# Performance work log

Hardware: AMD Instinct MI355X
Metric: run time of the kernel (lower is better)

The kernel has to match this reference:

```python
import jax, jax.numpy as jnp
import numpy as np

B, T, K = 64, 1024, 128
START, STOP = K - 2, K - 1  # tag_dictionary['<START>'], tag_dictionary['<STOP>']
NEG = -10000.0


def setup_inputs() -> dict:
    key = jax.random.key(0)
    k1, k2, k3, k4 = jax.random.split(key, 4)
    feats = jax.random.normal(k1, (B, T, K), jnp.float32)
    tags = jax.random.randint(k2, (B, T), 0, K - 2)          # real labels only
    lens = jax.random.randint(k3, (B,), 1, T + 1)            # 1 <= len <= T
    transitions = jax.random.normal(k4, (K, K), jnp.float32)
    transitions = transitions.at[START, :].set(NEG).at[:, STOP].set(NEG)
    return {"feats": feats, "tags": tags, "lens": lens, "transitions": transitions}


def _forward_alg(feats, transitions, lens):
    # feats: [B, T, K]; CRF forward (log-partition) via scan over time.
    B_, T_, K_ = feats.shape
    # init: only START position kept from feats[:, 0, :], rest -10000
    alpha0 = jnp.full((B_, K_), NEG, feats.dtype).at[:, START].set(feats[:, 0, START])

    def step(alpha, feat_i):
        # tag_var[b, s, p] = feat_i[b, s] + transitions[s, p] + alpha[b, p]
        new = feat_i + jax.scipy.special.logsumexp(alpha[:, None, :] + transitions[None, :, :], axis=2)
        return new, new

    _, alphas = jax.lax.scan(step, alpha0, jnp.swapaxes(feats[:, 1:, :], 0, 1))  # [T-1, B, K]
    all_alphas = jnp.concatenate([alpha0[None], alphas], axis=0)  # [T, B, K]; idx t-1 == forward_var[:, t]
    terminal = all_alphas[lens - 1, jnp.arange(B_)]               # [B, K]
    return jax.scipy.special.logsumexp(terminal, axis=1)          # [B]


def _score_sentence(feats, transitions, tags, lens):
    B_, T_, K_ = feats.shape
    pos = jnp.arange(T_ - 1)
    # pad_stop_tags = tags[:, 1:] with positions >= len-1 replaced by STOP
    stop_tags = jnp.where(pos[None, :] >= (lens - 1)[:, None], STOP, tags[:, 1:])
    trans_sc = transitions[stop_tags, tags[:, :-1]]               # [B, T-1]
    tmask = (pos[None, :] < (lens - 1)[:, None]).astype(feats.dtype)
    emit = jnp.take_along_axis(feats, tags[:, :, None], axis=2)[:, :, 0]  # [B, T]
    emask = (jnp.arange(T_)[None, :] < lens[:, None]).astype(feats.dtype)
    return jnp.sum(trans_sc * tmask, axis=1) + jnp.sum(emit * emask, axis=1)


def reference(feats, tags, lens, transitions):
    forward_score = _forward_alg(feats, transitions, lens)
    gold_score = _score_sentence(feats, transitions, tags, lens)
    return jnp.mean(forward_score - gold_score)
```

## Files before the change

kernel.cpp:

```cpp
#include <hip/hip_runtime.h>
#include <math.h>

#define BB 64
#define TT 1024
#define KK 128
#define START_TAG 126
#define STOP_TAG 127
#define NTHREADS 512
#define CS 64

typedef float v2f __attribute__((ext_vector_type(2)));

__global__ __launch_bounds__(NTHREADS) void crf_forward(
    const float* __restrict__ feats,
    const int*   __restrict__ tags,
    const int*   __restrict__ lens,
    const float* __restrict__ trans,
    float*       __restrict__ out_pb)
{
  __shared__ float Tld[KK][KK + 1];
  __shared__ __align__(16) float e_lds[KK];
  __shared__ float partial[NTHREADS];
  __shared__ float maxT_lds[KK];
  __shared__ __align__(16) float Fbuf[CS * KK];
  __shared__ float wsum[NTHREADS / 64];

  const int tid = threadIdx.x;
  const int b   = blockIdx.x;
  const int j   = tid & (KK - 1);
  const int q   = tid >> 7;
  const int L   = lens[b];
  const float* fb = feats + (size_t)b * TT * KK;

  for (int i = tid; i < KK * KK; i += NTHREADS)
    Tld[i >> 7][i & (KK - 1)] = trans[i];
  __syncthreads();

  float mT = -INFINITY;
  #pragma unroll
  for (int i = 0; i < 32; ++i) mT = fmaxf(mT, Tld[j][q * 32 + i]);
  partial[tid] = mT;
  __syncthreads();
  const float maxTj = fmaxf(fmaxf(partial[j], partial[j + 128]),
                            fmaxf(partial[j + 256], partial[j + 384]));
  v2f Er2[16];
  #pragma unroll
  for (int i = 0; i < 16; ++i) {
    Er2[i][0] = __expf(Tld[j][q * 32 + 2 * i]     - maxTj);
    Er2[i][1] = __expf(Tld[j][q * 32 + 2 * i + 1] - maxTj);
  }
  __syncthreads();
  if (q == 0) maxT_lds[j] = maxTj;

  if (tid < KK) e_lds[tid] = (tid == START_TAG) ? 1.0f : 0.0f;
  float M = fb[START_TAG];
  __syncthreads();

  const int j0 = (tid * 16) & (KK - 1);
  float4 mTv[4];
  #pragma unroll
  for (int i = 0; i < 4; ++i) mTv[i] = ((const float4*)maxT_lds)[(j0 >> 2) + i];

  float4 pf[4];
  {
    const float4* src = (const float4*)fb;
    #pragma unroll
    for (int i = 0; i < 4; ++i) pf[i] = src[tid * 4 + i];
  }

  for (int c = 0; c * CS < L; ++c) {
    float4* Fb4 = (float4*)Fbuf;
    #pragma unroll
    for (int i = 0; i < 4; ++i) {
      float4 v = pf[i];
      float4 m = mTv[i];
      float4 o;
      o.x = __expf(v.x + m.x); o.y = __expf(v.y + m.y);
      o.z = __expf(v.z + m.z); o.w = __expf(v.w + m.w);
      Fb4[tid * 4 + i] = o;
    }
    if ((c + 1) * CS < TT) {
      const float4* src = (const float4*)(fb + (size_t)(c + 1) * CS * KK);
      #pragma unroll
      for (int i = 0; i < 4; ++i) pf[i] = src[tid * 4 + i];
    }
    __syncthreads();

    const int t_begin = (c == 0) ? 1 : c * CS;
    const int t_end   = (L < (c + 1) * CS) ? L : (c + 1) * CS;
    for (int t = t_begin; t < t_end; ++t) {
      const v2f* e2 = (const v2f*)(e_lds + q * 32);
      v2f a0 = {0.f, 0.f}, a1 = {0.f, 0.f}, a2 = {0.f, 0.f}, a3 = {0.f, 0.f};
      #pragma unroll
      for (int i = 0; i < 4; ++i) {
        a0 += e2[4 * i + 0] * Er2[4 * i + 0];
        a1 += e2[4 * i + 1] * Er2[4 * i + 1];
        a2 += e2[4 * i + 2] * Er2[4 * i + 2];
        a3 += e2[4 * i + 3] * Er2[4 * i + 3];
      }
      v2f asum = (a0 + a1) + (a2 + a3);
      float F = Fbuf[(t & (CS - 1)) * KK + j];
      partial[tid] = asum[0] + asum[1];
      __syncthreads();

      if (q == 0) {
        float d = (partial[j]       + partial[j + 128]) +
                  (partial[j + 256] + partial[j + 384]);
        float s = (partial[START_TAG]       + partial[START_TAG + 128]) +
                  (partial[START_TAG + 256] + partial[START_TAG + 384]);
        float r;
        asm("v_rcp_f32 %0, %1" : "=v"(r) : "v"(s));
        e_lds[j] = d * F * r;
        if (tid < 64) M += __logf(s);
      }
      __syncthreads();
    }
  }

  float fwd = 0.f;
  if (tid < 64) {
    float sm = e_lds[tid] + e_lds[tid + 64];
    #pragma unroll
    for (int m = 1; m < 64; m <<= 1) sm += __shfl_xor(sm, m, 64);
    fwd = M + __logf(sm);
  }

  float g = 0.f;
  const int* tg = tags + b * TT;
  for (int t = tid; t < TT; t += NTHREADS) {
    if (t < L)     g += fb[(size_t)t * KK + tg[t]];
    if (t < L - 1) g += Tld[tg[t + 1]][tg[t]];
  }
  #pragma unroll
  for (int m = 1; m < 64; m <<= 1) g += __shfl_xor(g, m, 64);
  if ((tid & 63) == 0) wsum[tid >> 6] = g;
  __syncthreads();
  if (tid == 0) {
    float gold = 0.f;
    #pragma unroll
    for (int w = 0; w < NTHREADS / 64; ++w) gold += wsum[w];
    out_pb[b] = fwd - gold;
  }
}

__global__ void crf_mean(const float* __restrict__ pb, float* __restrict__ out) {
  int tid = threadIdx.x;
  float v = pb[tid];
  #pragma unroll
  for (int m = 1; m < 64; m <<= 1) v += __shfl_xor(v, m, 64);
  if (tid == 0) out[0] = v * (1.0f / 64.0f);
}

extern "C" void kernel_launch(void* const* d_in, const int* in_sizes, int n_in,
                              void* d_out, int out_size, void* d_ws, size_t ws_size,
                              hipStream_t stream) {
  const float* feats = (const float*)d_in[0];
  const int*   tags  = (const int*)d_in[1];
  const int*   lens  = (const int*)d_in[2];
  const float* trans = (const float*)d_in[3];
  float* pb = (float*)d_ws;
  crf_forward<<<BB, NTHREADS, 0, stream>>>(feats, tags, lens, trans, pb);
  crf_mean<<<1, 64, 0, stream>>>(pb, (float*)d_out);
}
```

Baseline: 450.3 us.

## Halve threads per row and double-buffer alpha to drop one barrier per step

Switches from four threads per tag with an LDS partial-sum reduction to two adjacent threads per tag combined by a wave shuffle. Alpha is double-buffered so each time step needs only one __syncthreads instead of two. The normaliser is now computed redundantly per thread as the sum of the previous alpha rather than read from the START-row partial. The cost is twice the per-thread dot-product length and register footprint (64 exp-transition values per thread), which may lengthen the serial per-step critical path.

```diff
diff --git a/kernel.cpp b/kernel.cpp
--- a/kernel.cpp
+++ b/kernel.cpp
@@ -6,7 +6,7 @@
 #define KK 128
 #define START_TAG 126
 #define STOP_TAG 127
-#define NTHREADS 512
+#define NTHREADS 256
 #define CS 64
 
 typedef float v2f __attribute__((ext_vector_type(2)));
@@ -19,16 +19,15 @@
     float*       __restrict__ out_pb)
 {
   __shared__ float Tld[KK][KK + 1];
-  __shared__ __align__(16) float e_lds[KK];
-  __shared__ float partial[NTHREADS];
-  __shared__ float maxT_lds[KK];
+  __shared__ __align__(16) float e_two[2][KK];
+  __shared__ __align__(16) float maxT_lds[KK];
   __shared__ __align__(16) float Fbuf[CS * KK];
   __shared__ float wsum[NTHREADS / 64];
 
   const int tid = threadIdx.x;
   const int b   = blockIdx.x;
-  const int j   = tid & (KK - 1);
-  const int q   = tid >> 7;
+  const int j   = tid >> 1;
+  const int h   = tid & 1;
   const int L   = lens[b];
   const float* fb = feats + (size_t)b * TT * KK;
 
@@ -38,88 +37,81 @@
 
   float mT = -INFINITY;
   #pragma unroll
-  for (int i = 0; i < 32; ++i) mT = fmaxf(mT, Tld[j][q * 32 + i]);
-  partial[tid] = mT;
-  __syncthreads();
-  const float maxTj = fmaxf(fmaxf(partial[j], partial[j + 128]),
-                            fmaxf(partial[j + 256], partial[j + 384]));
-  v2f Er2[16];
+  for (int i = 0; i < 64; ++i) mT = fmaxf(mT, Tld[j][h * 64 + i]);
+  mT = fmaxf(mT, __shfl_xor(mT, 1, 64));
+  v2f Er2[32];
   #pragma unroll
-  for (int i = 0; i < 16; ++i) {
-    Er2[i][0] = __expf(Tld[j][q * 32 + 2 * i]     - maxTj);
-    Er2[i][1] = __expf(Tld[j][q * 32 + 2 * i + 1] - maxTj);
+  for (int i = 0; i < 32; ++i) {
+    Er2[i][0] = __expf(Tld[j][h * 64 + 2 * i]     - mT);
+    Er2[i][1] = __expf(Tld[j][h * 64 + 2 * i + 1] - mT);
   }
-  __syncthreads();
-  if (q == 0) maxT_lds[j] = maxTj;
+  if (h == 0) maxT_lds[j] = mT;
 
-  if (tid < KK) e_lds[tid] = (tid == START_TAG) ? 1.0f : 0.0f;
+  if (tid < KK) e_two[0][tid] = (tid == START_TAG) ? 1.0f : 0.0f;
   float M = fb[START_TAG];
   __syncthreads();
 
-  const int j0 = (tid * 16) & (KK - 1);
-  float4 mTv[4];
-  #pragma unroll
-  for (int i = 0; i < 4; ++i) mTv[i] = ((const float4*)maxT_lds)[(j0 >> 2) + i];
+  const float4 mTv = ((const float4*)maxT_lds)[tid & 31];
 
-  float4 pf[4];
+  float4 pf[8];
   {
     const float4* src = (const float4*)fb;
     #pragma unroll
-    for (int i = 0; i < 4; ++i) pf[i] = src[tid * 4 + i];
+    for (int i = 0; i < 8; ++i) pf[i] = src[i * NTHREADS + tid];
   }
 
+  int cur = 0;
   for (int c = 0; c * CS < L; ++c) {
     float4* Fb4 = (float4*)Fbuf;
     #pragma unroll
-    for (int i = 0; i < 4; ++i) {
+    for (int i = 0; i < 8; ++i) {
       float4 v = pf[i];
-      float4 m = mTv[i];
       float4 o;
-      o.x = __expf(v.x + m.x); o.y = __expf(v.y + m.y);
-      o.z = __expf(v.z + m.z); o.w = __expf(v.w + m.w);
-      Fb4[tid * 4 + i] = o;
+      o.x = __expf(v.x + mTv.x); o.y = __expf(v.y + mTv.y);
+      o.z = __expf(v.z + mTv.z); o.w = __expf(v.w + mTv.w);
+      Fb4[i * NTHREADS + tid] = o;
     }
     if ((c + 1) * CS < TT) {
       const float4* src = (const float4*)(fb + (size_t)(c + 1) * CS * KK);
       #pragma unroll
-      for (int i = 0; i < 4; ++i) pf[i] = src[tid * 4 + i];
+      for (int i = 0; i < 8; ++i) pf[i] = src[i * NTHREADS + tid];
     }
     __syncthreads();
 
-    const int t_begin = (c == 0) ? 1 : c * CS;
-    const int t_end   = (L < (c + 1) * CS) ? L : (c + 1) * CS;
-    for (int t = t_begin; t < t_end; ++t) {
-      const v2f* e2 = (const v2f*)(e_lds + q * 32);
-      v2f a0 = {0.f, 0.f}, a1 = {0.f, 0.f}, a2 = {0.f, 0.f}, a3 = {0.f, 0.f};
+    const int t0 = (c == 0) ? 1 : c * CS;
+    const int t1 = (L < (c + 1) * CS) ? L : (c + 1) * CS;
+    for (int t = t0; t < t1; ++t) {
+      const v2f* e2 = (const v2f*)(e_two[cur] + h * 64);
+      v2f a0 = {0.f,0.f}, a1 = {0.f,0.f}, a2 = {0.f,0.f}, a3 = {0.f,0.f};
+      v2f s0 = {0.f,0.f}, s1 = {0.f,0.f}, s2 = {0.f,0.f}, s3 = {0.f,0.f};
       #pragma unroll
-      for (int i = 0; i < 4; ++i) {
-        a0 += e2[4 * i + 0] * Er2[4 * i + 0];
-        a1 += e2[4 * i + 1] * Er2[4 * i + 1];
-        a2 += e2[4 * i + 2] * Er2[4 * i + 2];
-        a3 += e2[4 * i + 3] * Er2[4 * i + 3];
+      for (int i = 0; i < 8; ++i) {
+        v2f ev0 = e2[4 * i + 0], ev1 = e2[4 * i + 1];
+        v2f ev2 = e2[4 * i + 2], ev3 = e2[4 * i + 3];
+        a0 += ev0 * Er2[4 * i + 0];  s0 += ev0;
+        a1 += ev1 * Er2[4 * i + 1];  s1 += ev1;
+        a2 += ev2 * Er2[4 * i + 2];  s2 += ev2;
+        a3 += ev3 * Er2[4 * i + 3];  s3 += ev3;
       }
-      v2f asum = (a0 + a1) + (a2 + a3);
-      float F = Fbuf[(t & (CS - 1)) * KK + j];
-      partial[tid] = asum[0] + asum[1];
-      __syncthreads();
-
-      if (q == 0) {
-        float d = (partial[j]       + partial[j + 128]) +
-                  (partial[j + 256] + partial[j + 384]);
-        float s = (partial[START_TAG]       + partial[START_TAG + 128]) +
-                  (partial[START_TAG + 256] + partial[START_TAG + 384]);
-        float r;
-        asm("v_rcp_f32 %0, %1" : "=v"(r) : "v"(s));
-        e_lds[j] = d * F * r;
-        if (tid < 64) M += __logf(s);
-      }
+      v2f av = (a0 + a1) + (a2 + a3);
+      v2f sv = (s0 + s1) + (s2 + s3);
+      float p  = av[0] + av[1];
+      float sg = sv[0] + sv[1];
+      float F  = Fbuf[(t & (CS - 1)) * KK + j];
+      p  += __shfl_xor(p, 1, 64);
+      sg += __shfl_xor(sg, 1, 64);
+      float r;
+      asm("v_rcp_f32 %0, %1" : "=v"(r) : "v"(sg));
+      if (h == 0) e_two[cur ^ 1][j] = p * F * r;
+      if (tid < 64) M += __logf(sg);
+      cur ^= 1;
       __syncthreads();
     }
   }
 
   float fwd = 0.f;
   if (tid < 64) {
-    float sm = e_lds[tid] + e_lds[tid + 64];
+    float sm = e_two[cur][tid] + e_two[cur][tid + 64];
     #pragma unroll
     for (int m = 1; m < 64; m <<= 1) sm += __shfl_xor(sm, m, 64);
     fwd = M + __logf(sm);
```

New measurement: 619.3 us. +37.5%, slower.
